# Performance work log

Hardware: AMD Instinct MI355X
Metric: run time of the kernel (lower is better)

## Reference

```python
import jax, jax.numpy as jnp
import numpy as np

N_TOKENS = 8192
TOP_K = 2
N_EXPERTS = 8
D_IN = 2048
D_OUT = 2048


def setup_inputs() -> dict:
    key = jax.random.key(0)
    k1, k2, k3, k4 = jax.random.split(key, 4)
    inputs = jax.random.normal(k1, (N_TOKENS, D_IN), dtype=jnp.float32)
    # stored as [E, out, in], matching nn.Parameter(torch.empty(E, output_size, input_size))
    expert_weights = 0.02 * jax.random.normal(k2, (N_EXPERTS, D_OUT, D_IN), dtype=jnp.float32)
    gates = jax.nn.softmax(jax.random.normal(k3, (N_TOKENS, TOP_K), dtype=jnp.float32), axis=-1)
    # per (token, slot) expert assignment, then sort by expert as the router would
    flat_experts = jax.random.randint(k4, (N_TOKENS * TOP_K,), 0, N_EXPERTS, dtype=jnp.int32)
    sorted_scattered_idxs = jnp.argsort(flat_experts).astype(jnp.int32)
    sorted_expert_idxs = flat_experts[sorted_scattered_idxs]
    expert_offsets = jnp.cumsum(jnp.bincount(flat_experts, length=N_EXPERTS)).astype(jnp.int32)
    return {
        "inputs": inputs,
        "expert_weights": expert_weights,
        "gates": gates,
        "k": TOP_K,
        "sorted_expert_idxs": sorted_expert_idxs,
        "sorted_scattered_idxs": sorted_scattered_idxs,
        "expert_offsets": expert_offsets,
    }


def reference(inputs, expert_weights, gates, k, sorted_expert_idxs, sorted_scattered_idxs, expert_offsets):
    N, d_in = inputs.shape
    E = expert_weights.shape[0]
    Nk = N * k
    # forward permutes weight [E, out, in] -> [E, in, out]
    W = jnp.transpose(expert_weights, (0, 2, 1))
    d_out = W.shape[-1]
    # invert the sort: expert id for each flat (token, slot) index
    expert_per_flat = jnp.zeros((Nk,), dtype=sorted_expert_idxs.dtype).at[
        sorted_scattered_idxs].set(sorted_expert_idxs)
    # scatter2scatter: out_flat[j] = x[j // k] @ W[expert_per_flat[j]]
    x_rep = jnp.repeat(inputs, k, axis=0)  # [N*k, d_in]
    out_flat = jnp.zeros((Nk, d_out), dtype=inputs.dtype)
    for e in range(E):  # small fixed expert count; masked grouped GEMM
        mask = (expert_per_flat == e)[:, None]
        out_flat = out_flat + jnp.where(mask, x_rep, 0.0) @ W[e]
    # combine: (gates.unsqueeze(1) @ output_expanded).squeeze(1)
    out = jnp.einsum('nk,nkd->nd', gates, out_flat.reshape(N, k, d_out))
    return out
```

## Files before the change

### kernel.cpp

```cpp
#include <hip/hip_runtime.h>
#include <hip/hip_bf16.h>
#include <stdint.h>

#define NTOK   8192
#define TOPK   2
#define NEXP   8
#define DIN    2048
#define DOUT   2048
#define NK     (NTOK*TOPK)

#define BM 256
#define BN 128
#define BK 32

typedef __bf16 bf16_8 __attribute__((ext_vector_type(8)));
typedef float  f32x4  __attribute__((ext_vector_type(4)));

__device__ __forceinline__ void gl2lds16(const void* g, void* l) {
  auto gp = reinterpret_cast<const __attribute__((address_space(1))) uint32_t*>(
      reinterpret_cast<uintptr_t>(g));
  auto lp = reinterpret_cast<__attribute__((address_space(3))) uint32_t*>(
      reinterpret_cast<uintptr_t>(l));
  __builtin_amdgcn_global_load_lds(gp, lp, 16, 0, 0);
}

__global__ void cvt_all(const float4* __restrict__ w, uint4* __restrict__ wD,
                        const float4* __restrict__ x, uint4* __restrict__ xD,
                        int nW) {
  int b = blockIdx.x;
  const float4* src;
  uint4* dst;
  int i;
  if (b < nW) { src = w; dst = wD; i = b * 256 + threadIdx.x; }
  else        { src = x; dst = xD; i = (b - nW) * 256 + threadIdx.x; }
  float4 a0 = src[2 * i];
  float4 a1 = src[2 * i + 1];
  union { __bf16 h[8]; uint4 u; } r;
  r.h[0] = (__bf16)a0.x; r.h[1] = (__bf16)a0.y; r.h[2] = (__bf16)a0.z; r.h[3] = (__bf16)a0.w;
  r.h[4] = (__bf16)a1.x; r.h[5] = (__bf16)a1.y; r.h[6] = (__bf16)a1.z; r.h[7] = (__bf16)a1.w;
  dst[i] = r.u;
}

__global__ __launch_bounds__(512, 4)
void moe_gemm(const __bf16* __restrict__ X,
              const __bf16* __restrict__ W,
              const int* __restrict__ ssi,
              const int* __restrict__ offs,
              __bf16* __restrict__ flat)
{
  __shared__ __bf16 lA[2][BM * BK];
  __shared__ __bf16 lB[2][BN * BK];
  __shared__ int   sTok[BM];
  __shared__ int   sF[BM];

  const int tid = threadIdx.x;
  const int bid = blockIdx.x;
  const int nt  = bid & 15;
  const int mtg = bid >> 4;

  int start = 0, end = 0, e, cum = 0, prev = 0, mloc = 0, found = 0;
  for (e = 0; e < NEXP; ++e) {
    int oe  = offs[e];
    int seg = oe - prev;
    int t   = (seg + BM - 1) >> 8;
    if (mtg < cum + t) { start = prev; end = oe; mloc = mtg - cum; found = 1; break; }
    cum += t; prev = oe;
  }
  if (!found) return;

  const int m0 = start + mloc * BM;

  if (tid < BM) {
    int p     = m0 + tid;
    int valid = p < end;
    int f     = ssi[valid ? p : (end - 1)];
    sTok[tid] = f >> 1;
    sF[tid]   = valid ? f : -1;
  }
  __syncthreads();

  const int rs = tid >> 2;
  const int kc = (tid & 3) ^ ((tid >> 3) & 3);
  const __bf16* pA0 = X + (size_t)sTok[rs]       * DIN + kc * 8;
  const __bf16* pA1 = X + (size_t)sTok[rs + 128] * DIN + kc * 8;
  const __bf16* wB  = W + (size_t)e * DOUT * DIN + (size_t)(nt * BN) * DIN;
  const __bf16* pB0 = wB + (size_t)rs * DIN + kc * 8;
  char* ldsAb = (char*)lA + (tid >> 6) * 1024;
  char* ldsBb = (char*)lB + (tid >> 6) * 1024;

  const int w   = tid >> 6;
  const int l   = tid & 63;
  const int wm  = w >> 1, wn = w & 1;
  const int lr  = l & 15;
  const int kq  = l >> 4;
  const int kqs = kq ^ ((lr >> 1) & 3);
  const __bf16* aBase = (const __bf16*)lA + (wm * 64 + lr) * BK + kqs * 8;
  const __bf16* bBase = (const __bf16*)lB + (wn * 64 + lr) * BK + kqs * 8;

  gl2lds16(pA0, ldsAb);
  gl2lds16(pA1, ldsAb + 8192);
  gl2lds16(pB0, ldsBb);
  pA0 += BK; pA1 += BK; pB0 += BK;

  f32x4 acc[4][4] = {};

  for (int it = 0; it < DIN / BK; ++it) {
    const int cur = it & 1;
    __syncthreads();
    if (it < DIN / BK - 1) {
      const int nb = cur ^ 1;
      gl2lds16(pA0, ldsAb + nb * 16384);
      gl2lds16(pA1, ldsAb + nb * 16384 + 8192);
      gl2lds16(pB0, ldsBb + nb * 8192);
      pA0 += BK; pA1 += BK; pB0 += BK;
    }

    const __bf16* aB = aBase + cur * (BM * BK);
    const __bf16* bB = bBase + cur * (BN * BK);
    bf16_8 af[4], bf[4];
#pragma unroll
    for (int am = 0; am < 4; ++am) af[am] = *(const bf16_8*)(aB + am * 512);
#pragma unroll
    for (int bn = 0; bn < 4; ++bn) bf[bn] = *(const bf16_8*)(bB + bn * 512);
#pragma unroll
    for (int am = 0; am < 4; ++am)
#pragma unroll
      for (int bn = 0; bn < 4; ++bn)
        acc[am][bn] = __builtin_amdgcn_mfma_f32_16x16x32_bf16(
            af[am], bf[bn], acc[am][bn], 0, 0, 0);
  }

  const int colBase = nt * BN + wn * 64 + lr;
  const int rq = kq * 4;
#pragma unroll
  for (int am = 0; am < 4; ++am) {
#pragma unroll
    for (int v = 0; v < 4; ++v) {
      int rl = wm * 64 + am * 16 + rq + v;
      int f  = sF[rl];
      if (f < 0) continue;
      __bf16* row = flat + (size_t)f * DOUT + colBase;
#pragma unroll
      for (int bn = 0; bn < 4; ++bn)
        row[bn * 16] = (__bf16)acc[am][bn][v];
    }
  }
}

__global__ __launch_bounds__(256)
void combine(const __bf16* __restrict__ flat, const float* __restrict__ gates,
             float* __restrict__ out) {
  const int n = blockIdx.x;
  const int c = threadIdx.x * 8;
  bf16_8 y0 = *(const bf16_8*)(flat + (size_t)(2 * n)     * DOUT + c);
  bf16_8 y1 = *(const bf16_8*)(flat + (size_t)(2 * n + 1) * DOUT + c);
  const float2 g = *(const float2*)(gates + 2 * n);
  float o[8];
#pragma unroll
  for (int j = 0; j < 8; ++j)
    o[j] = g.x * (float)y0[j] + g.y * (float)y1[j];
  float4* dst = (float4*)(out + (size_t)n * DOUT + c);
  dst[0] = *(float4*)&o[0];
  dst[1] = *(float4*)&o[4];
}

extern "C" void kernel_launch(void* const* d_in, const int* in_sizes, int n_in,
                              void* d_out, int out_size, void* d_ws, size_t ws_size,
                              hipStream_t stream) {
  const float* inputs = (const float*)d_in[0];
  const float* ew     = (const float*)d_in[1];
  const float* gates  = (const float*)d_in[2];
  const int*   ssi    = (const int*)d_in[5];
  const int*   offs   = (const int*)d_in[6];
  float* out = (float*)d_out;

  __bf16* wsW = (__bf16*)d_ws;
  __bf16* wsX = wsW + (size_t)NEXP * DOUT * DIN;
  __bf16* wsF = wsX + (size_t)NTOK * DIN;

  const int n8w = NEXP * DOUT * DIN / 8;
  const int n8x = NTOK * DIN / 8;
  const int nWb = n8w / 256, nXb = n8x / 256;
  cvt_all<<<nWb + nXb, 256, 0, stream>>>((const float4*)ew, (uint4*)wsW,
                                         (const float4*)inputs, (uint4*)wsX, nWb);

  moe_gemm<<<72 * 16, 512, 0, stream>>>(wsX, wsW, ssi, offs, wsF);
  combine<<<NTOK, 256, 0, stream>>>(wsF, gates, out);
}
```

Baseline: 447.2 us.

## Enlarge MoE GEMM tile to 256x256 with triple-buffered LDS pipeline

Doubles the N tile to 256 so each of the 8 waves computes a 128x64 sub-tile (32 accumulators), halving the grid. It replaces the double-buffered loop with a three-stage LDS ring: loads run two tiles ahead and are guarded by explicit vmcnt waits. MFMA blocks are split into two halves with barriers and s_setprio to interleave LDS reads and compute. The aim is to improve arithmetic intensity and hide load latency, at the cost of higher register/LDS use, occupancy capped at 2, and fewer blocks (576) for 256 CUs, which risks a wave-quantization tail.

```diff
diff --git a/kernel.cpp b/kernel.cpp
--- a/kernel.cpp
+++ b/kernel.cpp
@@ -10,8 +10,13 @@
 #define NK     (NTOK*TOPK)
 
 #define BM 256
-#define BN 128
+#define BN 256
 #define BK 32
+#define KTILES   (DIN/BK)
+#define ABYTES   (BM*BK*2)
+#define BBYTES   (BN*BK*2)
+#define BUFBYTES (ABYTES+BBYTES)
+#define NBUF 3
 
 typedef __bf16 bf16_8 __attribute__((ext_vector_type(8)));
 typedef float  f32x4  __attribute__((ext_vector_type(4)));
@@ -41,22 +46,21 @@
   dst[i] = r.u;
 }
 
-__global__ __launch_bounds__(512, 4)
+__global__ __launch_bounds__(512, 2)
 void moe_gemm(const __bf16* __restrict__ X,
               const __bf16* __restrict__ W,
               const int* __restrict__ ssi,
               const int* __restrict__ offs,
               __bf16* __restrict__ flat)
 {
-  __shared__ __bf16 lA[2][BM * BK];
-  __shared__ __bf16 lB[2][BN * BK];
-  __shared__ int   sTok[BM];
-  __shared__ int   sF[BM];
+  __shared__ char lds[NBUF * BUFBYTES];
+  __shared__ int  sTok[BM];
+  __shared__ int  sF[BM];
 
   const int tid = threadIdx.x;
   const int bid = blockIdx.x;
-  const int nt  = bid & 15;
-  const int mtg = bid >> 4;
+  const int nt  = bid & 7;
+  const int mtg = bid >> 3;
 
   int start = 0, end = 0, e, cum = 0, prev = 0, mloc = 0, found = 0;
   for (e = 0; e < NEXP; ++e) {
@@ -83,60 +87,87 @@
   const int kc = (tid & 3) ^ ((tid >> 3) & 3);
   const __bf16* pA0 = X + (size_t)sTok[rs]       * DIN + kc * 8;
   const __bf16* pA1 = X + (size_t)sTok[rs + 128] * DIN + kc * 8;
-  const __bf16* wB  = W + (size_t)e * DOUT * DIN + (size_t)(nt * BN) * DIN;
-  const __bf16* pB0 = wB + (size_t)rs * DIN + kc * 8;
-  char* ldsAb = (char*)lA + (tid >> 6) * 1024;
-  char* ldsBb = (char*)lB + (tid >> 6) * 1024;
+  const __bf16* wBp = W + (size_t)e * DOUT * DIN + (size_t)(nt * BN) * DIN;
+  const __bf16* pB0 = wBp + (size_t)rs * DIN + kc * 8;
+  const __bf16* pB1 = wBp + (size_t)(rs + 128) * DIN + kc * 8;
+  char* wsl = (char*)lds + (tid >> 6) * 1024;
+
+  gl2lds16(pA0, wsl);           gl2lds16(pA1, wsl + 8192);
+  gl2lds16(pB0, wsl + 16384);   gl2lds16(pB1, wsl + 24576);
+  pA0 += BK; pA1 += BK; pB0 += BK; pB1 += BK;
+  gl2lds16(pA0, wsl + BUFBYTES);          gl2lds16(pA1, wsl + BUFBYTES + 8192);
+  gl2lds16(pB0, wsl + BUFBYTES + 16384);  gl2lds16(pB1, wsl + BUFBYTES + 24576);
+  pA0 += BK; pA1 += BK; pB0 += BK; pB1 += BK;
 
   const int w   = tid >> 6;
   const int l   = tid & 63;
-  const int wm  = w >> 1, wn = w & 1;
+  const int wm  = w >> 2, wn = w & 3;
   const int lr  = l & 15;
   const int kq  = l >> 4;
   const int kqs = kq ^ ((lr >> 1) & 3);
-  const __bf16* aBase = (const __bf16*)lA + (wm * 64 + lr) * BK + kqs * 8;
-  const __bf16* bBase = (const __bf16*)lB + (wn * 64 + lr) * BK + kqs * 8;
-
-  gl2lds16(pA0, ldsAb);
-  gl2lds16(pA1, ldsAb + 8192);
-  gl2lds16(pB0, ldsBb);
-  pA0 += BK; pA1 += BK; pB0 += BK;
-
-  f32x4 acc[4][4] = {};
-
-  for (int it = 0; it < DIN / BK; ++it) {
-    const int cur = it & 1;
-    __syncthreads();
-    if (it < DIN / BK - 1) {
-      const int nb = cur ^ 1;
-      gl2lds16(pA0, ldsAb + nb * 16384);
-      gl2lds16(pA1, ldsAb + nb * 16384 + 8192);
-      gl2lds16(pB0, ldsBb + nb * 8192);
-      pA0 += BK; pA1 += BK; pB0 += BK;
+  const char* aBase = (const char*)lds + (wm * 128 + lr) * 64 + kqs * 16;
+  const char* bBase = (const char*)lds + ABYTES + (wn * 64 + lr) * 64 + kqs * 16;
+
+  asm volatile("s_waitcnt vmcnt(4)" ::: "memory");
+  __builtin_amdgcn_s_barrier();
+
+  f32x4 acc[8][4] = {};
+  int rOff = 0;
+  int sOff = 2 * BUFBYTES;
+
+  for (int t = 0; t < KTILES; ++t) {
+    const char* aB = aBase + rOff;
+    const char* bB = bBase + rOff;
+
+    bf16_8 af[4], bf[4];
+#pragma unroll
+    for (int i = 0; i < 4; ++i) af[i] = *(const bf16_8*)(aB + i * 1024);
+#pragma unroll
+    for (int i = 0; i < 4; ++i) bf[i] = *(const bf16_8*)(bB + i * 1024);
+    if (t < KTILES - 2) {
+      char* d = wsl + sOff;
+      gl2lds16(pA0, d);           gl2lds16(pA1, d + 8192);
+      gl2lds16(pB0, d + 16384);   gl2lds16(pB1, d + 24576);
+      pA0 += BK; pA1 += BK; pB0 += BK; pB1 += BK;
     }
-
-    const __bf16* aB = aBase + cur * (BM * BK);
-    const __bf16* bB = bBase + cur * (BN * BK);
-    bf16_8 af[4], bf[4];
-#pragma unroll
-    for (int am = 0; am < 4; ++am) af[am] = *(const bf16_8*)(aB + am * 512);
-#pragma unroll
-    for (int bn = 0; bn < 4; ++bn) bf[bn] = *(const bf16_8*)(bB + bn * 512);
+    __builtin_amdgcn_s_barrier();
+    __builtin_amdgcn_s_setprio(1);
 #pragma unroll
     for (int am = 0; am < 4; ++am)
 #pragma unroll
       for (int bn = 0; bn < 4; ++bn)
         acc[am][bn] = __builtin_amdgcn_mfma_f32_16x16x32_bf16(
             af[am], bf[bn], acc[am][bn], 0, 0, 0);
+    __builtin_amdgcn_s_setprio(0);
+    __builtin_amdgcn_s_barrier();
+
+    bf16_8 ag[4];
+#pragma unroll
+    for (int i = 0; i < 4; ++i) ag[i] = *(const bf16_8*)(aB + 4096 + i * 1024);
+    if (t < KTILES - 2)       { asm volatile("s_waitcnt vmcnt(4)" ::: "memory"); }
+    else if (t == KTILES - 2) { asm volatile("s_waitcnt vmcnt(0)" ::: "memory"); }
+    __builtin_amdgcn_s_barrier();
+    __builtin_amdgcn_s_setprio(1);
+#pragma unroll
+    for (int am = 0; am < 4; ++am)
+#pragma unroll
+      for (int bn = 0; bn < 4; ++bn)
+        acc[am + 4][bn] = __builtin_amdgcn_mfma_f32_16x16x32_bf16(
+            ag[am], bf[bn], acc[am + 4][bn], 0, 0, 0);
+    __builtin_amdgcn_s_setprio(0);
+    __builtin_amdgcn_s_barrier();
+
+    rOff = (rOff == (NBUF - 1) * BUFBYTES) ? 0 : rOff + BUFBYTES;
+    sOff = (sOff == (NBUF - 1) * BUFBYTES) ? 0 : sOff + BUFBYTES;
   }
 
   const int colBase = nt * BN + wn * 64 + lr;
   const int rq = kq * 4;
 #pragma unroll
-  for (int am = 0; am < 4; ++am) {
+  for (int am = 0; am < 8; ++am) {
 #pragma unroll
     for (int v = 0; v < 4; ++v) {
-      int rl = wm * 64 + am * 16 + rq + v;
+      int rl = wm * 128 + am * 16 + rq + v;
       int f  = sF[rl];
       if (f < 0) continue;
       __bf16* row = flat + (size_t)f * DOUT + colBase;
@@ -184,6 +215,6 @@
   cvt_all<<<nWb + nXb, 256, 0, stream>>>((const float4*)ew, (uint4*)wsW,
                                          (const float4*)inputs, (uint4*)wsX, nWb);
 
-  moe_gemm<<<72 * 16, 512, 0, stream>>>(wsX, wsW, ssi, offs, wsF);
+  moe_gemm<<<72 * 8, 512, 0, stream>>>(wsX, wsW, ssi, offs, wsF);
   combine<<<NTOK, 256, 0, stream>>>(wsF, gates, out);
 }
```

Result: no change. 452.1 us (+1.1%).

## Triple-buffer LDS tiles with explicit vmcnt waits in MoE GEMM

Applied to the files above, without the earlier changes.

Replaces the double-buffered A/B LDS tiles with a three-slot ring buffer that prefetches two K-tiles ahead. Uses manual s_waitcnt vmcnt counts and raw s_barrier instead of __syncthreads at the loop top, so the global-to-LDS copies overlap more MFMA work. This raises LDS use per block, which may lower occupancy. The hand-written wait counts must match the compiler's ordering of memory operations to stay correct.

```diff
diff --git a/kernel.cpp b/kernel.cpp
--- a/kernel.cpp
+++ b/kernel.cpp
@@ -12,6 +12,9 @@
 #define BM 256
 #define BN 128
 #define BK 32
+#define KTILES  (DIN/BK)
+#define SLOT    24576
+#define NBUF    3
 
 typedef __bf16 bf16_8 __attribute__((ext_vector_type(8)));
 typedef float  f32x4  __attribute__((ext_vector_type(4)));
@@ -48,10 +51,9 @@
               const int* __restrict__ offs,
               __bf16* __restrict__ flat)
 {
-  __shared__ __bf16 lA[2][BM * BK];
-  __shared__ __bf16 lB[2][BN * BK];
-  __shared__ int   sTok[BM];
-  __shared__ int   sF[BM];
+  __shared__ char lds[NBUF * SLOT];
+  __shared__ int  sTok[BM];
+  __shared__ int  sF[BM];
 
   const int tid = threadIdx.x;
   const int bid = blockIdx.x;
@@ -83,10 +85,16 @@
   const int kc = (tid & 3) ^ ((tid >> 3) & 3);
   const __bf16* pA0 = X + (size_t)sTok[rs]       * DIN + kc * 8;
   const __bf16* pA1 = X + (size_t)sTok[rs + 128] * DIN + kc * 8;
-  const __bf16* wB  = W + (size_t)e * DOUT * DIN + (size_t)(nt * BN) * DIN;
-  const __bf16* pB0 = wB + (size_t)rs * DIN + kc * 8;
-  char* ldsAb = (char*)lA + (tid >> 6) * 1024;
-  char* ldsBb = (char*)lB + (tid >> 6) * 1024;
+  const __bf16* wBp = W + (size_t)e * DOUT * DIN + (size_t)(nt * BN) * DIN;
+  const __bf16* pB0 = wBp + (size_t)rs * DIN + kc * 8;
+  char* wsl = (char*)lds + (tid >> 6) * 1024;
+
+  gl2lds16(pA0, wsl);           gl2lds16(pA1, wsl + 8192);
+  gl2lds16(pB0, wsl + 16384);
+  pA0 += BK; pA1 += BK; pB0 += BK;
+  gl2lds16(pA0, wsl + SLOT);    gl2lds16(pA1, wsl + SLOT + 8192);
+  gl2lds16(pB0, wsl + SLOT + 16384);
+  pA0 += BK; pA1 += BK; pB0 += BK;
 
   const int w   = tid >> 6;
   const int l   = tid & 63;
@@ -94,40 +102,44 @@
   const int lr  = l & 15;
   const int kq  = l >> 4;
   const int kqs = kq ^ ((lr >> 1) & 3);
-  const __bf16* aBase = (const __bf16*)lA + (wm * 64 + lr) * BK + kqs * 8;
-  const __bf16* bBase = (const __bf16*)lB + (wn * 64 + lr) * BK + kqs * 8;
-
-  gl2lds16(pA0, ldsAb);
-  gl2lds16(pA1, ldsAb + 8192);
-  gl2lds16(pB0, ldsBb);
-  pA0 += BK; pA1 += BK; pB0 += BK;
+  const char* aBase = (const char*)lds + (wm * 64 + lr) * 64 + kqs * 16;
+  const char* bBase = (const char*)lds + 16384 + (wn * 64 + lr) * 64 + kqs * 16;
+
+  asm volatile("s_waitcnt vmcnt(3)" ::: "memory");
+  __builtin_amdgcn_s_barrier();
 
   f32x4 acc[4][4] = {};
-
-  for (int it = 0; it < DIN / BK; ++it) {
-    const int cur = it & 1;
-    __syncthreads();
-    if (it < DIN / BK - 1) {
-      const int nb = cur ^ 1;
-      gl2lds16(pA0, ldsAb + nb * 16384);
-      gl2lds16(pA1, ldsAb + nb * 16384 + 8192);
-      gl2lds16(pB0, ldsBb + nb * 8192);
+  int rOff = 0;
+  int sOff = 2 * SLOT;
+
+  for (int t = 0; t < KTILES; ++t) {
+    if (t < KTILES - 2) {
+      char* d = wsl + sOff;
+      gl2lds16(pA0, d);  gl2lds16(pA1, d + 8192);  gl2lds16(pB0, d + 16384);
       pA0 += BK; pA1 += BK; pB0 += BK;
+      sOff = (sOff == (NBUF - 1) * SLOT) ? 0 : sOff + SLOT;
     }
 
-    const __bf16* aB = aBase + cur * (BM * BK);
-    const __bf16* bB = bBase + cur * (BN * BK);
+    const char* aB = aBase + rOff;
+    const char* bB = bBase + rOff;
+    rOff = (rOff == (NBUF - 1) * SLOT) ? 0 : rOff + SLOT;
+
     bf16_8 af[4], bf[4];
 #pragma unroll
-    for (int am = 0; am < 4; ++am) af[am] = *(const bf16_8*)(aB + am * 512);
-#pragma unroll
-    for (int bn = 0; bn < 4; ++bn) bf[bn] = *(const bf16_8*)(bB + bn * 512);
+    for (int i = 0; i < 4; ++i) af[i] = *(const bf16_8*)(aB + i * 1024);
+#pragma unroll
+    for (int i = 0; i < 4; ++i) bf[i] = *(const bf16_8*)(bB + i * 1024);
+
 #pragma unroll
     for (int am = 0; am < 4; ++am)
 #pragma unroll
       for (int bn = 0; bn < 4; ++bn)
         acc[am][bn] = __builtin_amdgcn_mfma_f32_16x16x32_bf16(
             af[am], bf[bn], acc[am][bn], 0, 0, 0);
+
+    if (t < KTILES - 2)       { asm volatile("s_waitcnt vmcnt(3)" ::: "memory"); }
+    else if (t == KTILES - 2) { asm volatile("s_waitcnt vmcnt(0)" ::: "memory"); }
+    if (t < KTILES - 1) __builtin_amdgcn_s_barrier();
   }
 
   const int colBase = nt * BN + wn * 64 + lr;
```

New measurement: 437.0 us. 1.02x faster.
